# Performance work log

Hardware: AMD Instinct MI355X
Metric: run time of the kernel (lower is better)

## Reference

```python
import jax, jax.numpy as jnp
import numpy as np

# DenseAtt: att = sigmoid(Linear(concat(x_i, x_j))) * adj
# Linear over the concatenated pair decomposes exactly:
#   W @ [x_i; x_j] + b = (x_i @ W_left) + (x_j @ W_right) + b
# so we never materialize the (n, n, 2F) tensor. Same math, O(n^2) memory only.

N = 8192
F = 256

def setup_inputs() -> dict:
    key = jax.random.key(0)
    k1, k2, k3, k4 = jax.random.split(key, 4)
    x = jax.random.normal(k1, (N, F), dtype=jnp.float32)
    adj = jax.random.uniform(k2, (N, N), dtype=jnp.float32)
    # nn.Linear(2F, 1): weight [1, 2F], bias [1]. Store as W [2F, 1], b [1].
    bound = 1.0 / np.sqrt(2 * F)
    W = jax.random.uniform(k3, (2 * F, 1), dtype=jnp.float32, minval=-bound, maxval=bound)
    b = jax.random.uniform(k4, (1,), dtype=jnp.float32, minval=-bound, maxval=bound)
    return {"x": x, "adj": adj, "W": W, "b": b}


def reference(x, adj, W, b):
    # left scores: x @ W[:F]  -> [n, 1]; right scores: x @ W[F:] -> [n, 1]
    left = x @ W[:F]            # [n, 1]
    right = x @ W[F:]           # [n, 1]
    scores = left + right.T + b  # [n, n] == Linear(concat(x_i, x_j)).squeeze()
    att = jax.nn.sigmoid(scores)
    return adj * att
```

## Files before the change

### kernel.cpp

```cpp
#include <hip/hip_runtime.h>

#define NN 8192
#define FF 256

typedef float floatx4 __attribute__((ext_vector_type(4)));

__global__ void row_scores_kernel(const float* __restrict__ x,
                                  const float* __restrict__ W,
                                  const float* __restrict__ b,
                                  float* __restrict__ left,
                                  float* __restrict__ right) {
    const int row  = (int)((blockIdx.x * blockDim.x + threadIdx.x) >> 6);
    const int lane = (int)(threadIdx.x & 63);
    if (row >= NN) return;

    const floatx4 xv = reinterpret_cast<const floatx4*>(x + (size_t)row * FF)[lane];
    const floatx4 wl = reinterpret_cast<const floatx4*>(W)[lane];
    const floatx4 wr = reinterpret_cast<const floatx4*>(W + FF)[lane];

    float l = xv.x * wl.x + xv.y * wl.y + xv.z * wl.z + xv.w * wl.w;
    float r = xv.x * wr.x + xv.y * wr.y + xv.z * wr.z + xv.w * wr.w;

    #pragma unroll
    for (int off = 32; off; off >>= 1) {
        l += __shfl_down(l, off, 64);
        r += __shfl_down(r, off, 64);
    }
    if (lane == 0) {
        left[row]  = l + b[0];
        right[row] = r;
    }
}

#define K2_THREADS (2048u * 256u)
#define ILP 4

__device__ __forceinline__ float sigmoid_fast(float s) {
    return __builtin_amdgcn_rcpf(1.0f + __expf(-s));
}

__global__ __launch_bounds__(256) void att_kernel(const float* __restrict__ adj,
                                                  const float* __restrict__ left,
                                                  const float* __restrict__ right,
                                                  float* __restrict__ out) {
    const unsigned tid = blockIdx.x * 256u + threadIdx.x;
    const floatx4* __restrict__ adj4   = reinterpret_cast<const floatx4*>(adj);
    const floatx4* __restrict__ right4 = reinterpret_cast<const floatx4*>(right);
    floatx4* __restrict__ out4         = reinterpret_cast<floatx4*>(out);

    #pragma unroll
    for (int it = 0; it < 8; ++it) {
        unsigned idx[ILP];
        floatx4 a[ILP], r[ILP];
        float   li[ILP];

        #pragma unroll
        for (int k = 0; k < ILP; ++k) {
            idx[k] = tid + (unsigned)(it * ILP + k) * K2_THREADS;
            a[k]   = __builtin_nontemporal_load(&adj4[idx[k]]);
        }
        #pragma unroll
        for (int k = 0; k < ILP; ++k) {
            const unsigned i  = idx[k] >> 11;
            const unsigned j4 = idx[k] & 2047u;
            li[k] = left[i];
            r[k]  = right4[j4];
        }

        #pragma unroll
        for (int k = 0; k < ILP; ++k) {
            floatx4 o;
            o.x = a[k].x * sigmoid_fast(li[k] + r[k].x);
            o.y = a[k].y * sigmoid_fast(li[k] + r[k].y);
            o.z = a[k].z * sigmoid_fast(li[k] + r[k].z);
            o.w = a[k].w * sigmoid_fast(li[k] + r[k].w);
            __builtin_nontemporal_store(o, &out4[idx[k]]);
        }
    }
}

extern "C" void kernel_launch(void* const* d_in, const int* in_sizes, int n_in,
                              void* d_out, int out_size, void* d_ws, size_t ws_size,
                              hipStream_t stream) {
    const float* x   = (const float*)d_in[0];
    const float* adj = (const float*)d_in[1];
    const float* W   = (const float*)d_in[2];
    const float* b   = (const float*)d_in[3];
    float* out = (float*)d_out;

    float* left  = (float*)d_ws;
    float* right = left + NN;

    row_scores_kernel<<<dim3((NN * 64) / 256), dim3(256), 0, stream>>>(x, W, b, left, right);

    att_kernel<<<dim3(2048), dim3(256), 0, stream>>>(adj, left, right, out);
}
```

Measured before the change: 117.4 us.

## Assign rows per block and keep right scores in registers

Restructures the attention kernel so each block processes four contiguous rows, with each thread loading its slice of the right-score vector once into registers and reusing it across rows. This removes the repeated per-element gathers of left/right scores and the index div/mod arithmetic. It also drops the nontemporal load/store hints, so adj and output traffic now goes through the normal cache path, which may change bandwidth behaviour.

```diff
diff --git a/kernel.cpp b/kernel.cpp
--- a/kernel.cpp
+++ b/kernel.cpp
@@ -32,49 +32,48 @@
     }
 }
 
-#define K2_THREADS (2048u * 256u)
-#define ILP 4
-
 __device__ __forceinline__ float sigmoid_fast(float s) {
     return __builtin_amdgcn_rcpf(1.0f + __expf(-s));
 }
+
+#define ROWS_PER_BLOCK 4
+#define Q_PER_ROW (NN / 4 / 256)
 
 __global__ __launch_bounds__(256) void att_kernel(const float* __restrict__ adj,
                                                   const float* __restrict__ left,
                                                   const float* __restrict__ right,
                                                   float* __restrict__ out) {
-    const unsigned tid = blockIdx.x * 256u + threadIdx.x;
+    const unsigned t  = threadIdx.x;
+    const unsigned r0 = blockIdx.x * ROWS_PER_BLOCK;
+
     const floatx4* __restrict__ adj4   = reinterpret_cast<const floatx4*>(adj);
     const floatx4* __restrict__ right4 = reinterpret_cast<const floatx4*>(right);
     floatx4* __restrict__ out4         = reinterpret_cast<floatx4*>(out);
 
+    floatx4 rq[Q_PER_ROW];
     #pragma unroll
-    for (int it = 0; it < 8; ++it) {
-        unsigned idx[ILP];
-        floatx4 a[ILP], r[ILP];
-        float   li[ILP];
+    for (int q = 0; q < Q_PER_ROW; ++q)
+        rq[q] = right4[t + (unsigned)q * 256u];
 
+    float lrow[ROWS_PER_BLOCK];
+    #pragma unroll
+    for (int k = 0; k < ROWS_PER_BLOCK; ++k)
+        lrow[k] = left[r0 + k];
+
+    #pragma unroll
+    for (int k = 0; k < ROWS_PER_BLOCK; ++k) {
+        const unsigned rowbase = (r0 + k) * (NN / 4);
+        const float li = lrow[k];
         #pragma unroll
-        for (int k = 0; k < ILP; ++k) {
-            idx[k] = tid + (unsigned)(it * ILP + k) * K2_THREADS;
-            a[k]   = __builtin_nontemporal_load(&adj4[idx[k]]);
-        }
-        #pragma unroll
-        for (int k = 0; k < ILP; ++k) {
-            const unsigned i  = idx[k] >> 11;
-            const unsigned j4 = idx[k] & 2047u;
-            li[k] = left[i];
-            r[k]  = right4[j4];
-        }
-
-        #pragma unroll
-        for (int k = 0; k < ILP; ++k) {
+        for (int q = 0; q < Q_PER_ROW; ++q) {
+            const unsigned idx = rowbase + t + (unsigned)q * 256u;
+            const floatx4 a = adj4[idx];
             floatx4 o;
-            o.x = a[k].x * sigmoid_fast(li[k] + r[k].x);
-            o.y = a[k].y * sigmoid_fast(li[k] + r[k].y);
-            o.z = a[k].z * sigmoid_fast(li[k] + r[k].z);
-            o.w = a[k].w * sigmoid_fast(li[k] + r[k].w);
-            __builtin_nontemporal_store(o, &out4[idx[k]]);
+            o.x = a.x * sigmoid_fast(li + rq[q].x);
+            o.y = a.y * sigmoid_fast(li + rq[q].y);
+            o.z = a.z * sigmoid_fast(li + rq[q].z);
+            o.w = a.w * sigmoid_fast(li + rq[q].w);
+            out4[idx] = o;
         }
     }
 }
@@ -93,5 +92,5 @@
 
     row_scores_kernel<<<dim3((NN * 64) / 256), dim3(256), 0, stream>>>(x, W, b, left, right);
 
-    att_kernel<<<dim3(2048), dim3(256), 0, stream>>>(adj, left, right, out);
+    att_kernel<<<dim3(NN / ROWS_PER_BLOCK), dim3(256), 0, stream>>>(adj, left, right, out);
 }
```

New measurement: 112.2 us. 4.4% less time.
